# Performance work log

Hardware: AMD Instinct MI355X
Metric: run time of the kernel (lower is better)

The kernel has to match this reference:

```python
import jax, jax.numpy as jnp
import numpy as np

GRID_SIZE = 3
LN_EPS = 1e-5
BASIS_EPS = 1e-6


def setup_inputs() -> dict:
    key = jax.random.key(0)
    ks = jax.random.split(key, 5)
    B, S, D_IN, D_OUT, SE_H = 8, 1024, 1024, 1024, 32
    x = jax.random.normal(ks[0], (B, S, D_IN), dtype=jnp.float32)
    base_weight = jax.random.normal(ks[1], (D_OUT, D_IN), dtype=jnp.float32) * 0.01
    spline_weight = jax.random.normal(ks[2], (D_OUT, D_IN, GRID_SIZE), dtype=jnp.float32) * 0.005
    ln_w = jnp.ones((D_OUT,), dtype=jnp.float32)
    ln_b = jnp.zeros((D_OUT,), dtype=jnp.float32)
    se_w1 = jax.random.normal(ks[3], (SE_H, D_OUT), dtype=jnp.float32) * 0.03
    se_b1 = jnp.zeros((SE_H,), dtype=jnp.float32)
    se_w2 = jax.random.normal(ks[4], (D_OUT, SE_H), dtype=jnp.float32) * 0.03
    se_b2 = jnp.zeros((D_OUT,), dtype=jnp.float32)
    return {"x": x, "base_weight": base_weight, "spline_weight": spline_weight,
            "ln_w": ln_w, "ln_b": ln_b, "se_w1": se_w1, "se_b1": se_b1,
            "se_w2": se_w2, "se_b2": se_b2}


def _kan_layer(x2d, base_weight, spline_weight, ln_w, ln_b, se_w1, se_b1, se_w2, se_b2):
    # x2d: [N, D_in]
    base = x2d @ base_weight.T                                   # [N, D_out]
    grid = jnp.linspace(-1.0, 1.0, GRID_SIZE).astype(x2d.dtype)  # [G]
    dist = jnp.abs(x2d[..., None] - grid)                        # [N, D_in, G]
    basis = jnp.where(dist < 1.0, (1.0 - dist) ** 2, 0.0)
    basis = basis / (basis.sum(axis=-1, keepdims=True) + BASIS_EPS)
    spline = jnp.einsum('nig,oig->no', basis, spline_weight)     # [N, D_out]
    out = base + spline
    # LayerNorm (dropout is identity at inference)
    mu = out.mean(axis=-1, keepdims=True)
    var = ((out - mu) ** 2).mean(axis=-1, keepdims=True)
    out = (out - mu) * jax.lax.rsqrt(var + LN_EPS) * ln_w + ln_b
    # SE gating (2D branch: applied per flattened token)
    h = jnp.maximum(out @ se_w1.T + se_b1, 0.0)
    se = jax.nn.sigmoid(h @ se_w2.T + se_b2)
    return out * se


def reference(x, base_weight, spline_weight, ln_w, ln_b, se_w1, se_b1, se_w2, se_b2):
    B, S, D = x.shape
    out = _kan_layer(x.reshape(-1, D), base_weight, spline_weight,
                     ln_w, ln_b, se_w1, se_b1, se_w2, se_b2)
    return out.reshape(B, S, -1)
```

## Files before the change

### kernel.cpp

```cpp
#include <hip/hip_runtime.h>
#include <hip/hip_bf16.h>
#include <math.h>

typedef __attribute__((ext_vector_type(8))) __bf16 bf16x8;
typedef __attribute__((ext_vector_type(4))) float f32x4;

#define NTOK 8192
#define DIN 1024
#define DOUT 1024
#define KAUG 4096
#define SEH 32

#define BK 64
#define KHALF 2048
#define NKT (KHALF / BK)

static __device__ __forceinline__ unsigned short f2bf(float f) {
  union { float f; unsigned u; } v; v.f = f;
  unsigned r = (v.u + 0x7FFFu + ((v.u >> 16) & 1u)) >> 16;
  return (unsigned short)r;
}

__global__ __launch_bounds__(256) void build_aaug(const float* __restrict__ x,
                                                  ushort* __restrict__ Aaug) {
  const int id = blockIdx.x * 256 + threadIdx.x;
  const float v = x[id];
  const float d0 = fabsf(v + 1.f), d1 = fabsf(v), d2 = fabsf(v - 1.f);
  float b0 = (d0 < 1.f) ? (1.f - d0) * (1.f - d0) : 0.f;
  float b1 = (d1 < 1.f) ? (1.f - d1) * (1.f - d1) : 0.f;
  float b2 = (d2 < 1.f) ? (1.f - d2) * (1.f - d2) : 0.f;
  const float inv = 1.f / (b0 + b1 + b2 + 1e-6f);
  ushort4 o;
  o.x = f2bf(v);
  o.y = f2bf(b0 * inv);
  o.z = f2bf(b1 * inv);
  o.w = f2bf(b2 * inv);
  ((ushort4*)Aaug)[id] = o;
}

__global__ __launch_bounds__(256) void pack_w(const float* __restrict__ bw,
                                              const float* __restrict__ sw,
                                              ushort* __restrict__ Waug) {
  const int id = blockIdx.x * 256 + threadIdx.x;
  ushort4 o;
  o.x = f2bf(bw[id]);
  o.y = f2bf(sw[id * 3 + 0]);
  o.z = f2bf(sw[id * 3 + 1]);
  o.w = f2bf(sw[id * 3 + 2]);
  ((ushort4*)Waug)[id] = o;
}

__global__ __launch_bounds__(256) void pack_se(const float* __restrict__ w1,
                                               const float* __restrict__ w2,
                                               ushort* __restrict__ w1b,
                                               ushort* __restrict__ w2b) {
  const int id = blockIdx.x * 256 + threadIdx.x;
  if (id < SEH * DOUT) w1b[id] = f2bf(w1[id]);
  else w2b[id - SEH * DOUT] = f2bf(w2[id - SEH * DOUT]);
}

#define WAITVM(N) asm volatile("s_waitcnt vmcnt(" #N ")" ::: "memory")

__global__ __launch_bounds__(512, 2) void gemm_sk(const ushort* __restrict__ A,
                                                  const ushort* __restrict__ B,
                                                  float* __restrict__ P0,
                                                  float* __restrict__ P1) {
  __shared__ ushort As[2][256 * BK];
  __shared__ ushort Bs[2][256 * BK];
  const int tid = threadIdx.x;
  const int wid = tid >> 6, lane = tid & 63;
  const int l16 = lane & 15, lk = lane >> 4;
  const int wm = wid >> 2, wn = wid & 3;

  const int g = (blockIdx.x & 7) * 32 + (blockIdx.x >> 3);
  const int kh = g >> 7;
  const int bm = (g & 127) >> 2;
  const int bn = g & 3;

  const ushort* Ab = A + (size_t)bm * 256 * KAUG + kh * KHALF;
  const ushort* Bb = B + (size_t)bn * 256 * KAUG + kh * KHALF;
  float* P = kh ? P1 : P0;

  const int lrow = lane >> 3;
  const int lcb = (lane & 7) ^ lrow;

  f32x4 acc[8][4] = {};

#define STAGE_A(kt, buf, r)                                                     \
  __builtin_amdgcn_global_load_lds(                                             \
      (const __attribute__((address_space(1))) void*)(Ab +                      \
          (size_t)((r) * 64 + wid * 8 + lrow) * KAUG + (kt) * BK + lcb * 8),    \
      (__attribute__((address_space(3))) void*)(&As[buf][((r) * 512 + wid * 64) * 8]), \
      16, 0, 0)
#define STAGE_B(kt, buf, r)                                                     \
  __builtin_amdgcn_global_load_lds(                                             \
      (const __attribute__((address_space(1))) void*)(Bb +                      \
          (size_t)((r) * 64 + wid * 8 + lrow) * KAUG + (kt) * BK + lcb * 8),    \
      (__attribute__((address_space(3))) void*)(&Bs[buf][((r) * 512 + wid * 64) * 8]), \
      16, 0, 0)
#define STAGE_ALL(kt, buf)                                                      \
  do {                                                                          \
    STAGE_A(kt, buf, 0); STAGE_A(kt, buf, 1); STAGE_A(kt, buf, 2); STAGE_A(kt, buf, 3); \
    STAGE_B(kt, buf, 0); STAGE_B(kt, buf, 1); STAGE_B(kt, buf, 2); STAGE_B(kt, buf, 3); \
  } while (0)

#define RD_A(buf, m, kk) \
  (*(const bf16x8*)&As[buf][(wm * 128 + (m) * 16 + l16) * 64 + ((((kk) * 4 + lk) ^ (l16 & 7)) << 3)])
#define RD_B(buf, n, kk) \
  (*(const bf16x8*)&Bs[buf][(wn * 64 + (n) * 16 + l16) * 64 + ((((kk) * 4 + lk) ^ (l16 & 7)) << 3)])

  STAGE_ALL(0, 0);

  int bc = 0;
  for (int kt = 0; kt < NKT; ++kt) {
    if (kt < NKT - 1) {
      STAGE_ALL(kt + 1, bc ^ 1);
      WAITVM(8);
    } else {
      WAITVM(0);
    }
    __builtin_amdgcn_s_barrier();
    __builtin_amdgcn_sched_barrier(0);

    bf16x8 af[8][2], bfr[4][2];
#pragma unroll
    for (int m = 0; m < 8; ++m) { af[m][0] = RD_A(bc, m, 0); af[m][1] = RD_A(bc, m, 1); }
#pragma unroll
    for (int n = 0; n < 4; ++n) { bfr[n][0] = RD_B(bc, n, 0); bfr[n][1] = RD_B(bc, n, 1); }

    __builtin_amdgcn_s_setprio(1);
#pragma unroll
    for (int k2 = 0; k2 < 2; ++k2)
#pragma unroll
      for (int m = 0; m < 8; ++m)
#pragma unroll
        for (int n = 0; n < 4; ++n)
          acc[m][n] = __builtin_amdgcn_mfma_f32_16x16x32_bf16(af[m][k2], bfr[n][k2], acc[m][n], 0, 0, 0);
    __builtin_amdgcn_s_setprio(0);

    __builtin_amdgcn_s_barrier();
    bc ^= 1;
  }

  float* Cb = P + (size_t)(bm * 256 + wm * 128) * DOUT + bn * 256 + wn * 64;
#pragma unroll
  for (int m = 0; m < 8; ++m)
#pragma unroll
    for (int n = 0; n < 4; ++n)
#pragma unroll
      for (int j = 0; j < 4; ++j)
        Cb[(size_t)(m * 16 + lk * 4 + j) * DOUT + n * 16 + l16] = acc[m][n][j];
}

__global__ __launch_bounds__(256) void ln_se_mfma(
    float* __restrict__ out, const float* __restrict__ p1,
    const float* __restrict__ ln_w, const float* __restrict__ ln_b,
    const ushort* __restrict__ w1b, const float* __restrict__ se_b1,
    const ushort* __restrict__ w2b, const float* __restrict__ se_b2) {
  __shared__ float Yl[16 * 1028];
  __shared__ float Hpart[4][512];
  __shared__ unsigned Hb[256];
  const int tid = threadIdx.x;
  const int w = tid >> 6, lane = tid & 63;
  const int l16 = lane & 15, lk = lane >> 4;
  const int tok0 = blockIdx.x * 16;

  float lw[16], lb[16];
#pragma unroll
  for (int e = 0; e < 16; ++e) {
    lw[e] = ln_w[e * 64 + lane];
    lb[e] = ln_b[e * 64 + lane];
  }

  for (int q = 0; q < 4; ++q) {
    const int tl = w * 4 + q;
    const float* r0 = out + (size_t)(tok0 + tl) * DOUT;
    const float* r1 = p1 + (size_t)(tok0 + tl) * DOUT;
    float v[16];
#pragma unroll
    for (int e = 0; e < 16; ++e) v[e] = r0[e * 64 + lane] + r1[e * 64 + lane];
    float s = 0.f, ss = 0.f;
#pragma unroll
    for (int e = 0; e < 16; ++e) { s += v[e]; ss += v[e] * v[e]; }
#pragma unroll
    for (int m = 32; m; m >>= 1) { s += __shfl_xor(s, m); ss += __shfl_xor(ss, m); }
    const float mu = s * (1.f / (float)DOUT);
    const float inv = rsqrtf(ss * (1.f / (float)DOUT) - mu * mu + 1e-5f);
#pragma unroll
    for (int e = 0; e < 16; ++e)
      Yl[tl * 1028 + e * 64 + lane] = (v[e] - mu) * inv * lw[e] + lb[e];
  }
  __syncthreads();

  f32x4 acc1[2] = {};
#pragma unroll
  for (int s = 0; s < 8; ++s) {
    const int ks = w * 8 + s;
    const int k = ks * 32 + lk * 8;
    const float* yp = &Yl[l16 * 1028 + k];
    const f32x4 q0 = *(const f32x4*)yp;
    const f32x4 q1 = *(const f32x4*)(yp + 4);
    bf16x8 af;
    af[0] = (__bf16)q0[0]; af[1] = (__bf16)q0[1];
    af[2] = (__bf16)q0[2]; af[3] = (__bf16)q0[3];
    af[4] = (__bf16)q1[0]; af[5] = (__bf16)q1[1];
    af[6] = (__bf16)q1[2]; af[7] = (__bf16)q1[3];
#pragma unroll
    for (int nt = 0; nt < 2; ++nt) {
      const bf16x8 bf = *(const bf16x8*)(w1b + (nt * 16 + l16) * 1024 + ks * 32 + lk * 8);
      acc1[nt] = __builtin_amdgcn_mfma_f32_16x16x32_bf16(af, bf, acc1[nt], 0, 0, 0);
    }
  }
#pragma unroll
  for (int nt = 0; nt < 2; ++nt)
#pragma unroll
    for (int j = 0; j < 4; ++j)
      Hpart[w][(lk * 4 + j) * 32 + nt * 16 + l16] = acc1[nt][j];
  __syncthreads();

  {
    const int e2 = tid * 2;
    float h0 = Hpart[0][e2] + Hpart[1][e2] + Hpart[2][e2] + Hpart[3][e2];
    float h1 = Hpart[0][e2 + 1] + Hpart[1][e2 + 1] + Hpart[2][e2 + 1] + Hpart[3][e2 + 1];
    h0 = fmaxf(h0 + se_b1[e2 & 31], 0.f);
    h1 = fmaxf(h1 + se_b1[(e2 & 31) + 1], 0.f);
    Hb[tid] = (unsigned)f2bf(h0) | ((unsigned)f2bf(h1) << 16);
  }
  __syncthreads();

  union { uint4 u; bf16x8 v; } ha;
  ha.u = *(const uint4*)&Hb[l16 * 16 + lk * 4];
  const int nbase = w * 256;
#pragma unroll
  for (int nt = 0; nt < 16; ++nt) {
    const int col = nbase + nt * 16 + l16;
    const bf16x8 bf = *(const bf16x8*)(w2b + col * 32 + lk * 8);
    f32x4 gz = {0.f, 0.f, 0.f, 0.f};
    gz = __builtin_amdgcn_mfma_f32_16x16x32_bf16(ha.v, bf, gz, 0, 0, 0);
    const float b2 = se_b2[col];
#pragma unroll
    for (int j = 0; j < 4; ++j) {
      const int tl = lk * 4 + j;
      const float sg = 1.f / (1.f + __expf(-(gz[j] + b2)));
      out[(size_t)(tok0 + tl) * DOUT + col] = Yl[tl * 1028 + col] * sg;
    }
  }
}

extern "C" void kernel_launch(void* const* d_in, const int* in_sizes, int n_in,
                              void* d_out, int out_size, void* d_ws, size_t ws_size,
                              hipStream_t stream) {
  const float* x = (const float*)d_in[0];
  const float* bw = (const float*)d_in[1];
  const float* sw = (const float*)d_in[2];
  const float* ln_w = (const float*)d_in[3];
  const float* ln_b = (const float*)d_in[4];
  const float* se_w1 = (const float*)d_in[5];
  const float* se_b1 = (const float*)d_in[6];
  const float* se_w2 = (const float*)d_in[7];
  const float* se_b2 = (const float*)d_in[8];
  float* out = (float*)d_out;

  ushort* Aaug = (ushort*)d_ws;
  ushort* Waug = Aaug + (size_t)NTOK * KAUG;
  ushort* w1b = Waug + (size_t)DOUT * KAUG;
  ushort* w2b = w1b + SEH * DOUT;
  float* P1 = (float*)(w2b + SEH * DOUT);

  build_aaug<<<NTOK * DIN / 256, 256, 0, stream>>>(x, Aaug);
  pack_w<<<DOUT * DIN / 256, 256, 0, stream>>>(bw, sw, Waug);
  pack_se<<<2 * SEH * DOUT / 256, 256, 0, stream>>>(se_w1, se_w2, w1b, w2b);
  gemm_sk<<<256, 512, 0, stream>>>(Aaug, Waug, out, P1);
  ln_se_mfma<<<NTOK / 16, 256, 0, stream>>>(out, P1, ln_w, ln_b, w1b, se_b1, w2b, se_b2);
}
```

Measured before the change: 120.0 us.

## Fuse spline basis feature construction into GEMM A-tile staging

Removes the separate build_aaug kernel and its 64MB bf16 augmented-activation buffer. The GEMM now loads fp32 x directly into registers, computes the basis features (using a fast reciprocal) and writes the swizzled bf16 A tile into LDS after the MFMA block, prefetching one tile ahead. This cuts a global write and re-read of the augmented matrix, but adds VALU work and register pressure inside the GEMM main loop, and each x element is recomputed once per column block (4 times).

```diff
diff --git a/kernel.cpp b/kernel.cpp
--- a/kernel.cpp
+++ b/kernel.cpp
@@ -21,21 +21,16 @@
   return (unsigned short)r;
 }
 
-__global__ __launch_bounds__(256) void build_aaug(const float* __restrict__ x,
-                                                  ushort* __restrict__ Aaug) {
-  const int id = blockIdx.x * 256 + threadIdx.x;
-  const float v = x[id];
+static __device__ __forceinline__ uint2 feat4(float v) {
   const float d0 = fabsf(v + 1.f), d1 = fabsf(v), d2 = fabsf(v - 1.f);
-  float b0 = (d0 < 1.f) ? (1.f - d0) * (1.f - d0) : 0.f;
-  float b1 = (d1 < 1.f) ? (1.f - d1) * (1.f - d1) : 0.f;
-  float b2 = (d2 < 1.f) ? (1.f - d2) * (1.f - d2) : 0.f;
-  const float inv = 1.f / (b0 + b1 + b2 + 1e-6f);
-  ushort4 o;
-  o.x = f2bf(v);
-  o.y = f2bf(b0 * inv);
-  o.z = f2bf(b1 * inv);
-  o.w = f2bf(b2 * inv);
-  ((ushort4*)Aaug)[id] = o;
+  const float b0 = (d0 < 1.f) ? (1.f - d0) * (1.f - d0) : 0.f;
+  const float b1 = (d1 < 1.f) ? (1.f - d1) * (1.f - d1) : 0.f;
+  const float b2 = (d2 < 1.f) ? (1.f - d2) * (1.f - d2) : 0.f;
+  const float inv = __builtin_amdgcn_rcpf(b0 + b1 + b2 + 1e-6f);
+  uint2 r;
+  r.x = (unsigned)f2bf(v) | ((unsigned)f2bf(b0 * inv) << 16);
+  r.y = (unsigned)f2bf(b1 * inv) | ((unsigned)f2bf(b2 * inv) << 16);
+  return r;
 }
 
 __global__ __launch_bounds__(256) void pack_w(const float* __restrict__ bw,
@@ -59,12 +54,12 @@
   else w2b[id - SEH * DOUT] = f2bf(w2[id - SEH * DOUT]);
 }
 
-#define WAITVM(N) asm volatile("s_waitcnt vmcnt(" #N ")" ::: "memory")
-
-__global__ __launch_bounds__(512, 2) void gemm_sk(const ushort* __restrict__ A,
-                                                  const ushort* __restrict__ B,
-                                                  float* __restrict__ P0,
-                                                  float* __restrict__ P1) {
+#define WAITVM_LG(N) asm volatile("s_waitcnt vmcnt(" #N ") lgkmcnt(0)" ::: "memory")
+
+__global__ __launch_bounds__(512, 2) void gemm_fused(const float* __restrict__ x,
+                                                     const ushort* __restrict__ B,
+                                                     float* __restrict__ P0,
+                                                     float* __restrict__ P1) {
   __shared__ ushort As[2][256 * BK];
   __shared__ ushort Bs[2][256 * BK];
   const int tid = threadIdx.x;
@@ -77,7 +72,7 @@
   const int bm = (g & 127) >> 2;
   const int bn = g & 3;
 
-  const ushort* Ab = A + (size_t)bm * 256 * KAUG + kh * KHALF;
+  const float* Xb = x + (size_t)bm * 256 * DIN + (size_t)kh * (KHALF / 4);
   const ushort* Bb = B + (size_t)bn * 256 * KAUG + kh * KHALF;
   float* P = kh ? P1 : P0;
 
@@ -86,38 +81,46 @@
 
   f32x4 acc[8][4] = {};
 
-#define STAGE_A(kt, buf, r)                                                     \
-  __builtin_amdgcn_global_load_lds(                                             \
-      (const __attribute__((address_space(1))) void*)(Ab +                      \
-          (size_t)((r) * 64 + wid * 8 + lrow) * KAUG + (kt) * BK + lcb * 8),    \
-      (__attribute__((address_space(3))) void*)(&As[buf][((r) * 512 + wid * 64) * 8]), \
-      16, 0, 0)
+#define XLOAD(kt, r) \
+  (*(const float2*)&Xb[(size_t)((r) * 64 + wid * 8 + lrow) * DIN + (kt) * 16 + lcb * 2])
+#define AWRITE(buf, r, xv)                                              \
+  do {                                                                  \
+    const uint2 f0 = feat4((xv).x), f1 = feat4((xv).y);                 \
+    uint4 wv; wv.x = f0.x; wv.y = f0.y; wv.z = f1.x; wv.w = f1.y;       \
+    *(uint4*)&As[buf][((r) * 512 + wid * 64 + lane) * 8] = wv;          \
+  } while (0)
+
 #define STAGE_B(kt, buf, r)                                                     \
   __builtin_amdgcn_global_load_lds(                                             \
       (const __attribute__((address_space(1))) void*)(Bb +                      \
           (size_t)((r) * 64 + wid * 8 + lrow) * KAUG + (kt) * BK + lcb * 8),    \
       (__attribute__((address_space(3))) void*)(&Bs[buf][((r) * 512 + wid * 64) * 8]), \
       16, 0, 0)
-#define STAGE_ALL(kt, buf)                                                      \
-  do {                                                                          \
-    STAGE_A(kt, buf, 0); STAGE_A(kt, buf, 1); STAGE_A(kt, buf, 2); STAGE_A(kt, buf, 3); \
-    STAGE_B(kt, buf, 0); STAGE_B(kt, buf, 1); STAGE_B(kt, buf, 2); STAGE_B(kt, buf, 3); \
-  } while (0)
+#define STAGE_B4(kt, buf)                                                       \
+  do { STAGE_B(kt, buf, 0); STAGE_B(kt, buf, 1); STAGE_B(kt, buf, 2); STAGE_B(kt, buf, 3); } while (0)
 
 #define RD_A(buf, m, kk) \
   (*(const bf16x8*)&As[buf][(wm * 128 + (m) * 16 + l16) * 64 + ((((kk) * 4 + lk) ^ (l16 & 7)) << 3)])
 #define RD_B(buf, n, kk) \
   (*(const bf16x8*)&Bs[buf][(wn * 64 + (n) * 16 + l16) * 64 + ((((kk) * 4 + lk) ^ (l16 & 7)) << 3)])
 
-  STAGE_ALL(0, 0);
+  {
+    float2 x0 = XLOAD(0, 0), x1 = XLOAD(0, 1), x2 = XLOAD(0, 2), x3 = XLOAD(0, 3);
+    STAGE_B4(0, 0);
+    AWRITE(0, 0, x0); AWRITE(0, 1, x1); AWRITE(0, 2, x2); AWRITE(0, 3, x3);
+  }
 
   int bc = 0;
   for (int kt = 0; kt < NKT; ++kt) {
-    if (kt < NKT - 1) {
-      STAGE_ALL(kt + 1, bc ^ 1);
-      WAITVM(8);
+    const bool pf = (kt < NKT - 1);
+    float2 xn0, xn1, xn2, xn3;
+    if (pf) {
+      xn0 = XLOAD(kt + 1, 0); xn1 = XLOAD(kt + 1, 1);
+      xn2 = XLOAD(kt + 1, 2); xn3 = XLOAD(kt + 1, 3);
+      STAGE_B4(kt + 1, bc ^ 1);
+      WAITVM_LG(8);
     } else {
-      WAITVM(0);
+      WAITVM_LG(0);
     }
     __builtin_amdgcn_s_barrier();
     __builtin_amdgcn_sched_barrier(0);
@@ -137,6 +140,11 @@
         for (int n = 0; n < 4; ++n)
           acc[m][n] = __builtin_amdgcn_mfma_f32_16x16x32_bf16(af[m][k2], bfr[n][k2], acc[m][n], 0, 0, 0);
     __builtin_amdgcn_s_setprio(0);
+
+    if (pf) {
+      AWRITE(bc ^ 1, 0, xn0); AWRITE(bc ^ 1, 1, xn1);
+      AWRITE(bc ^ 1, 2, xn2); AWRITE(bc ^ 1, 3, xn3);
+    }
 
     __builtin_amdgcn_s_barrier();
     bc ^= 1;
@@ -261,15 +269,13 @@
   const float* se_b2 = (const float*)d_in[8];
   float* out = (float*)d_out;
 
-  ushort* Aaug = (ushort*)d_ws;
-  ushort* Waug = Aaug + (size_t)NTOK * KAUG;
+  ushort* Waug = (ushort*)d_ws;
   ushort* w1b = Waug + (size_t)DOUT * KAUG;
   ushort* w2b = w1b + SEH * DOUT;
   float* P1 = (float*)(w2b + SEH * DOUT);
 
-  build_aaug<<<NTOK * DIN / 256, 256, 0, stream>>>(x, Aaug);
   pack_w<<<DOUT * DIN / 256, 256, 0, stream>>>(bw, sw, Waug);
   pack_se<<<2 * SEH * DOUT / 256, 256, 0, stream>>>(se_w1, se_w2, w1b, w2b);
-  gemm_sk<<<256, 512, 0, stream>>>(Aaug, Waug, out, P1);
+  gemm_fused<<<256, 512, 0, stream>>>(x, Waug, out, P1);
   ln_se_mfma<<<NTOK / 16, 256, 0, stream>>>(out, P1, ln_w, ln_b, w1b, se_b1, w2b, se_b2);
 }
```

Result: slower. 151.2 us (+26.0%).
